# Optimization experiments

Measured on AMD Instinct MI355X. Metric: run time of the kernel, lower is better.

## Reference

```python
import jax, jax.numpy as jnp
import numpy as np

N_NODES = 10000
N_EDGES = 320000
NFEAT, NHID, NCLASS = 512, 256, 40


def setup_inputs() -> dict:
    key = jax.random.key(0)
    ks = jax.random.split(key, 8)
    x = jax.random.normal(ks[0], (N_NODES, NFEAT), dtype=jnp.float32)
    edge_src = jax.random.randint(ks[1], (N_EDGES,), 0, N_NODES, dtype=jnp.int32)
    edge_dst = jax.random.randint(ks[2], (N_EDGES,), 0, N_NODES, dtype=jnp.int32)
    edge_w = jax.random.uniform(ks[3], (N_EDGES,), dtype=jnp.float32)
    W1 = jax.random.normal(ks[4], (NFEAT, NHID), dtype=jnp.float32) * (1.0 / np.sqrt(NFEAT))
    b1 = jax.random.normal(ks[5], (NHID,), dtype=jnp.float32) * 0.01
    W2 = jax.random.normal(ks[6], (NHID, NCLASS), dtype=jnp.float32) * (1.0 / np.sqrt(NHID))
    b2 = jax.random.normal(ks[7], (NCLASS,), dtype=jnp.float32) * 0.01
    return {"x": x, "edge_src": edge_src, "edge_dst": edge_dst, "edge_w": edge_w,
            "W1": W1, "b1": b1, "W2": W2, "b2": b2}


def _spmm(edge_src, edge_dst, edge_w, h):
    # out[i] = sum_{e: dst_e == i} w_e * h[src_e]   (sparse adj @ h)
    msgs = h[edge_src] * edge_w[:, None]            # [E, d]
    return jax.ops.segment_sum(msgs, edge_dst, num_segments=h.shape[0])


def reference(x, edge_src, edge_dst, edge_w, W1, b1, W2, b2):
    # Layer 1: GraphConvolution(nfeat->nhid) with ReLU (dropout = identity in eval)
    h = jax.nn.relu(_spmm(edge_src, edge_dst, edge_w, x @ W1) + b1)
    # Layer 2: GraphConvolution(nhid->nclass), identity activation
    out = _spmm(edge_src, edge_dst, edge_w, h @ W2) + b2
    return jax.nn.log_softmax(out, axis=1)
```

## Files before the change

### kernel.cpp

```cpp
#include <hip/hip_runtime.h>
#include <hip/hip_bf16.h>
#include <math.h>

#define N_NODES 10000
#define MPAD    10112
#define N_EDGES 320000
#define NFEAT   512
#define NHID    256
#define NCLASS  40
#define SLOT    96
#define EB      ((N_EDGES + 255) / 256)
#define G1X     (MPAD / 128)
#define NG1     (G1X * (NHID / 128))

typedef short  short8  __attribute__((ext_vector_type(8)));
typedef float  floatx4 __attribute__((ext_vector_type(4)));

__device__ __forceinline__ unsigned short f2b(float f) {
  __hip_bfloat16 h = __float2bfloat16(f);
  unsigned short u; __builtin_memcpy(&u, &h, 2); return u;
}
__device__ __forceinline__ float b2f(unsigned short u) {
  return __uint_as_float(((unsigned)u) << 16);
}
__device__ __forceinline__ short8 pack8(float4 a, float4 b) {
  short8 r;
  r[0] = (short)f2b(a.x); r[1] = (short)f2b(a.y); r[2] = (short)f2b(a.z); r[3] = (short)f2b(a.w);
  r[4] = (short)f2b(b.x); r[5] = (short)f2b(b.y); r[6] = (short)f2b(b.z); r[7] = (short)f2b(b.w);
  return r;
}


__global__ __launch_bounds__(256) void prep_k(const float* __restrict__ W1,
                                              const float* __restrict__ W2,
                                              unsigned short* __restrict__ w1t,
                                              unsigned short* __restrict__ w2t,
                                              int* __restrict__ cnt) {
  int tid = blockIdx.x * 256 + threadIdx.x;
  if (tid < N_NODES) cnt[tid] = 0;
  const int nw1 = NFEAT * NHID;
  if (tid < nw1) {
    int k = tid / NHID, n = tid % NHID;
    w1t[n * NFEAT + k] = f2b(W1[tid]);
  } else {
    int j = tid - nw1;
    if (j < 64 * NHID) {
      int n = j >> 8;
      int k = j & 255;
      w2t[j] = (n < NCLASS) ? f2b(W2[k * NCLASS + n]) : (unsigned short)0;
    }
  }
}


__global__ __launch_bounds__(256) void gemm1_scatter_k(
    const float* __restrict__ x, const unsigned short* __restrict__ w1t,
    unsigned short* __restrict__ xw1b,
    const int* __restrict__ src, const int* __restrict__ dst,
    const float* __restrict__ w, int* __restrict__ cnt, int2* __restrict__ epk) {
  if (blockIdx.x >= NG1) {
    int e = (blockIdx.x - NG1) * 256 + threadIdx.x;
    if (e < N_EDGES) {
      int d = dst[e];
      int p = atomicAdd(&cnt[d], 1);
      int2 pk; pk.x = src[e]; pk.y = __float_as_int(w[e]);
      epk[d * SLOT + p] = pk;
    }
    return;
  }
  __shared__ short8 As[128 * 4];
  __shared__ short8 Bs[128 * 4];

  const int b  = blockIdx.x;
  const int bx = b % G1X;
  const int by = b / G1X;
  const int bm = bx * 128;
  const int bn = by * 128;
  const int t  = threadIdx.x;
  const int l  = t & 63;
  const int wv = t >> 6;
  const int wr = wv >> 1, wc = wv & 1;

  const int rowX = t >> 1;
  const int sX   = (t & 1) * 2;

  const floatx4 zero = {0.f, 0.f, 0.f, 0.f};
  floatx4 acc[4][4];
#pragma unroll
  for (int mi = 0; mi < 4; mi++)
#pragma unroll
    for (int ni = 0; ni < 4; ni++) acc[mi][ni] = zero;

  const int q = l >> 4;

  for (int k0 = 0; k0 < NFEAT; k0 += 32) {
    int arow = bm + rowX;
    float4 xa0 = make_float4(0.f, 0.f, 0.f, 0.f), xa1 = xa0, xa2 = xa0, xa3 = xa0;
    if (arow < N_NODES) {
      const float* xp = &x[(size_t)arow * NFEAT + k0 + sX * 8];
      xa0 = *(const float4*)(xp);
      xa1 = *(const float4*)(xp + 4);
      xa2 = *(const float4*)(xp + 8);
      xa3 = *(const float4*)(xp + 12);
    }
    short8 a0 = pack8(xa0, xa1), a1 = pack8(xa2, xa3);
    short8 b0 = *(const short8*)&w1t[(size_t)(bn + rowX) * NFEAT + k0 + sX * 8];
    short8 b1v = *(const short8*)&w1t[(size_t)(bn + rowX) * NFEAT + k0 + sX * 8 + 8];
    __syncthreads();
    As[rowX * 4 + ((sX    ) ^ (rowX & 3))] = a0;
    As[rowX * 4 + ((sX + 1) ^ (rowX & 3))] = a1;
    Bs[rowX * 4 + ((sX    ) ^ (rowX & 3))] = b0;
    Bs[rowX * 4 + ((sX + 1) ^ (rowX & 3))] = b1v;
    __syncthreads();

    short8 af[4], bf[4];
#pragma unroll
    for (int mi = 0; mi < 4; mi++) {
      int ar = wr * 64 + mi * 16 + (l & 15);
      af[mi] = As[ar * 4 + (q ^ (ar & 3))];
    }
#pragma unroll
    for (int ni = 0; ni < 4; ni++) {
      int bc = wc * 64 + ni * 16 + (l & 15);
      bf[ni] = Bs[bc * 4 + (q ^ (bc & 3))];
    }
#pragma unroll
    for (int mi = 0; mi < 4; mi++)
#pragma unroll
      for (int ni = 0; ni < 4; ni++)
        acc[mi][ni] = __builtin_amdgcn_mfma_f32_16x16x32_bf16(af[mi], bf[ni], acc[mi][ni], 0, 0, 0);
  }

#pragma unroll
  for (int mi = 0; mi < 4; mi++)
#pragma unroll
    for (int ni = 0; ni < 4; ni++) {
      int row = bm + wr * 64 + mi * 16 + (l >> 4) * 4;
      int col = bn + wc * 64 + ni * 16 + (l & 15);
#pragma unroll
      for (int r = 0; r < 4; r++)
        xw1b[(size_t)(row + r) * NHID + col] = f2b(acc[mi][ni][r]);
    }
}


__global__ __launch_bounds__(256) void spmm1_k(const int* __restrict__ cnt,
                                               const int2* __restrict__ epk,
                                               const unsigned short* __restrict__ xw1b,
                                               const float* __restrict__ b1,
                                               unsigned short* __restrict__ h) {
  int bid     = blockIdx.x;
  int xcd     = bid & 7;
  int slice   = xcd >> 2;
  int quarter = xcd & 3;
  int wave    = threadIdx.x >> 6;
  int lane    = threadIdx.x & 63;
  int node    = (bid >> 3) * 4 + wave + quarter * 2500;
  int hh      = lane >> 5;
  int f       = lane & 31;
  int fbase   = slice * 128 + f * 4;

  int e0 = node * SLOT;
  int n  = cnt[node];
  float a0 = 0.f, a1 = 0.f, a2 = 0.f, a3 = 0.f;
  for (int base = 0; base < n; base += 64) {
    int c2 = n - base; if (c2 > 64) c2 = 64;
    int2 my = make_int2(0, 0);
    if (lane < c2) my = epk[e0 + base + lane];
    int j = 0;
    for (; j + 8 <= c2; j += 8) {
#pragma unroll
      for (int p = 0; p < 4; p++) {
        int   idx = j + 2 * p + hh;
        int   s   = __shfl(my.x, idx);
        float wj  = __int_as_float(__shfl(my.y, idx));
        uint2 v = *(const uint2*)&xw1b[(size_t)s * NHID + fbase];
        a0 = fmaf(wj, b2f((unsigned short)(v.x & 0xffff)), a0);
        a1 = fmaf(wj, b2f((unsigned short)(v.x >> 16)),    a1);
        a2 = fmaf(wj, b2f((unsigned short)(v.y & 0xffff)), a2);
        a3 = fmaf(wj, b2f((unsigned short)(v.y >> 16)),    a3);
      }
    }
    for (; j < c2; j++) {
      int   s  = __shfl(my.x, j);
      float wj = __int_as_float(__shfl(my.y, j));
      if (hh == 0) {
        uint2 v = *(const uint2*)&xw1b[(size_t)s * NHID + fbase];
        a0 = fmaf(wj, b2f((unsigned short)(v.x & 0xffff)), a0);
        a1 = fmaf(wj, b2f((unsigned short)(v.x >> 16)),    a1);
        a2 = fmaf(wj, b2f((unsigned short)(v.y & 0xffff)), a2);
        a3 = fmaf(wj, b2f((unsigned short)(v.y >> 16)),    a3);
      }
    }
  }
  a0 += __shfl_xor(a0, 32);
  a1 += __shfl_xor(a1, 32);
  a2 += __shfl_xor(a2, 32);
  a3 += __shfl_xor(a3, 32);
  if (hh == 0) {
    a0 = fmaxf(a0 + b1[fbase + 0], 0.f);
    a1 = fmaxf(a1 + b1[fbase + 1], 0.f);
    a2 = fmaxf(a2 + b1[fbase + 2], 0.f);
    a3 = fmaxf(a3 + b1[fbase + 3], 0.f);
    uint2 po;
    po.x = ((unsigned)f2b(a1) << 16) | f2b(a0);
    po.y = ((unsigned)f2b(a3) << 16) | f2b(a2);
    *(uint2*)&h[(size_t)node * NHID + fbase] = po;
  }
}


__global__ __launch_bounds__(256) void gemm2_k(const unsigned short* __restrict__ h,
                                               const unsigned short* __restrict__ w2t,
                                               float* __restrict__ hw2) {
  __shared__ short8 As[64 * 4];
  __shared__ short8 Bs[64 * 4];

  const int t  = threadIdx.x;
  const int bm = blockIdx.x * 64;
  const int l  = t & 63;
  const int wv = t >> 6;
  const int wr = wv >> 1, wc = wv & 1;
  const int srow = t >> 2, sslot = t & 3;

  const floatx4 zero = {0.f, 0.f, 0.f, 0.f};
  floatx4 acc[2][2];
  acc[0][0] = zero; acc[0][1] = zero; acc[1][0] = zero; acc[1][1] = zero;

  const int q = l >> 4;

  for (int k0 = 0; k0 < NHID; k0 += 32) {
    short8 av = *(const short8*)&h  [(size_t)(bm + srow) * NHID + k0 + sslot * 8];
    short8 bv = *(const short8*)&w2t[(size_t)srow * NHID + k0 + sslot * 8];
    __syncthreads();
    As[srow * 4 + (sslot ^ (srow & 3))] = av;
    Bs[srow * 4 + (sslot ^ (srow & 3))] = bv;
    __syncthreads();

    short8 af[2], bf2[2];
#pragma unroll
    for (int mi = 0; mi < 2; mi++) {
      int ar = wr * 32 + mi * 16 + (l & 15);
      af[mi] = As[ar * 4 + (q ^ (ar & 3))];
    }
#pragma unroll
    for (int ni = 0; ni < 2; ni++) {
      int bc = wc * 32 + ni * 16 + (l & 15);
      bf2[ni] = Bs[bc * 4 + (q ^ (bc & 3))];
    }
#pragma unroll
    for (int mi = 0; mi < 2; mi++)
#pragma unroll
      for (int ni = 0; ni < 2; ni++)
        acc[mi][ni] = __builtin_amdgcn_mfma_f32_16x16x32_bf16(af[mi], bf2[ni], acc[mi][ni], 0, 0, 0);
  }

#pragma unroll
  for (int mi = 0; mi < 2; mi++)
#pragma unroll
    for (int ni = 0; ni < 2; ni++) {
      int row = bm + wr * 32 + mi * 16 + (l >> 4) * 4;
      int col = wc * 32 + ni * 16 + (l & 15);
#pragma unroll
      for (int r = 0; r < 4; r++)
        hw2[(size_t)(row + r) * 64 + col] = acc[mi][ni][r];
    }
}


__global__ __launch_bounds__(256) void spmm2_k(const int* __restrict__ cnt,
                                               const int2* __restrict__ epk,
                                               const float* __restrict__ hw2,
                                               const float* __restrict__ b2,
                                               float* __restrict__ out) {
  int wave = threadIdx.x >> 6;
  int lane = threadIdx.x & 63;
  int i    = blockIdx.x * 4 + wave;
  int hh   = lane >> 5;
  int c    = lane & 31;
  bool act = (c * 2 < NCLASS);
  int e0 = i * SLOT;
  int n  = cnt[i];
  float a0 = 0.f, a1 = 0.f;
  for (int base = 0; base < n; base += 64) {
    int c2 = n - base; if (c2 > 64) c2 = 64;
    int2 my = make_int2(0, 0);
    if (lane < c2) my = epk[e0 + base + lane];
    int j = 0;
    for (; j + 8 <= c2; j += 8) {
#pragma unroll
      for (int p = 0; p < 4; p++) {
        int   idx = j + 2 * p + hh;
        int   s   = __shfl(my.x, idx);
        float wj  = __int_as_float(__shfl(my.y, idx));
        float2 v = *(const float2*)&hw2[(size_t)s * 64 + c * 2];
        a0 = fmaf(wj, v.x, a0);
        a1 = fmaf(wj, v.y, a1);
      }
    }
    for (; j < c2; j++) {
      int   s  = __shfl(my.x, j);
      float wj = __int_as_float(__shfl(my.y, j));
      if (hh == 0) {
        float2 v = *(const float2*)&hw2[(size_t)s * 64 + c * 2];
        a0 = fmaf(wj, v.x, a0);
        a1 = fmaf(wj, v.y, a1);
      }
    }
  }
  a0 += __shfl_xor(a0, 32);
  a1 += __shfl_xor(a1, 32);
  if (act) { a0 += b2[c * 2]; a1 += b2[c * 2 + 1]; }
  float mv = act ? fmaxf(a0, a1) : -INFINITY;
#pragma unroll
  for (int o = 16; o > 0; o >>= 1) mv = fmaxf(mv, __shfl_xor(mv, o));
  float ex = act ? (expf(a0 - mv) + expf(a1 - mv)) : 0.f;
#pragma unroll
  for (int o = 16; o > 0; o >>= 1) ex += __shfl_xor(ex, o);
  float ls = logf(ex);
  if (act && hh == 0) {
    float2 o2; o2.x = a0 - mv - ls; o2.y = a1 - mv - ls;
    *(float2*)&out[(size_t)i * NCLASS + c * 2] = o2;
  }
}


static inline size_t align256(size_t v) { return (v + 255) & ~(size_t)255; }

extern "C" void kernel_launch(void* const* d_in, const int* in_sizes, int n_in,
                              void* d_out, int out_size, void* d_ws, size_t ws_size,
                              hipStream_t stream) {
  const float* x        = (const float*)d_in[0];
  const int*   edge_src = (const int*)  d_in[1];
  const int*   edge_dst = (const int*)  d_in[2];
  const float* edge_w   = (const float*)d_in[3];
  const float* W1       = (const float*)d_in[4];
  const float* b1       = (const float*)d_in[5];
  const float* W2       = (const float*)d_in[6];
  const float* b2       = (const float*)d_in[7];
  float* out = (float*)d_out;

  char* ws = (char*)d_ws;
  size_t off = 0;
  unsigned short* w1t  = (unsigned short*)(ws + off); off = align256(off + (size_t)NFEAT * NHID * 2);
  unsigned short* w2t  = (unsigned short*)(ws + off); off = align256(off + (size_t)64 * NHID * 2);
  unsigned short* xw1b = (unsigned short*)(ws + off); off = align256(off + (size_t)MPAD * NHID * 2);
  unsigned short* h    = (unsigned short*)(ws + off); off = align256(off + (size_t)MPAD * NHID * 2);
  float* hw2 = (float*)(ws + off); off = align256(off + (size_t)MPAD * 64 * 4);
  int*   cnt = (int*)  (ws + off); off = align256(off + (size_t)N_NODES * 4);
  int2*  epk = (int2*) (ws + off); off = align256(off + (size_t)N_NODES * SLOT * 8);

  const int PREP_ITEMS = NFEAT * NHID + 64 * NHID;
  prep_k<<<(PREP_ITEMS + 255) / 256, 256, 0, stream>>>(W1, W2, w1t, w2t, cnt);

  gemm1_scatter_k<<<NG1 + EB, 256, 0, stream>>>(x, w1t, xw1b,
                                                edge_src, edge_dst, edge_w, cnt, epk);

  spmm1_k<<<5000, 256, 0, stream>>>(cnt, epk, xw1b, b1, h);

  gemm2_k<<<157, 256, 0, stream>>>(h, w2t, hw2);

  spmm2_k<<<2500, 256, 0, stream>>>(cnt, epk, hw2, b2, out);
}
```

Baseline: 78.55 us.

## Split edge scatter from GEMM1, pad atomic counters, double-buffer smaller GEMM tiles

Moves the edge scatter out of the fused GEMM1 launch into its own 1024-thread kernel. Per-node counters are padded to a 64-byte stride to reduce atomic contention and false sharing. GEMM1 now uses 64x128 tiles with double-buffered shared memory and register prefetch of the next K-slice, so one barrier per iteration replaces two and more blocks are launched. In exchange there is an extra kernel launch, the scatter no longer overlaps with GEMM work, and prep_k now launches over the larger padded counter range.

```diff
diff --git a/kernel.cpp b/kernel.cpp
--- a/kernel.cpp
+++ b/kernel.cpp
@@ -9,9 +9,8 @@
 #define NHID    256
 #define NCLASS  40
 #define SLOT    96
-#define EB      ((N_EDGES + 255) / 256)
-#define G1X     (MPAD / 128)
-#define NG1     (G1X * (NHID / 128))
+#define CSTRIDE 16
+#define NBM1    158
 
 typedef short  short8  __attribute__((ext_vector_type(8)));
 typedef float  floatx4 __attribute__((ext_vector_type(4)));
@@ -37,106 +36,115 @@
                                               unsigned short* __restrict__ w2t,
                                               int* __restrict__ cnt) {
   int tid = blockIdx.x * 256 + threadIdx.x;
-  if (tid < N_NODES) cnt[tid] = 0;
+  if (tid < N_NODES * CSTRIDE) cnt[tid] = 0;
   const int nw1 = NFEAT * NHID;
   if (tid < nw1) {
     int k = tid / NHID, n = tid % NHID;
     w1t[n * NFEAT + k] = f2b(W1[tid]);
-  } else {
+  } else if (tid < nw1 + 64 * NHID) {
     int j = tid - nw1;
-    if (j < 64 * NHID) {
-      int n = j >> 8;
-      int k = j & 255;
-      w2t[j] = (n < NCLASS) ? f2b(W2[k * NCLASS + n]) : (unsigned short)0;
-    }
-  }
-}
-
-
-__global__ __launch_bounds__(256) void gemm1_scatter_k(
-    const float* __restrict__ x, const unsigned short* __restrict__ w1t,
-    unsigned short* __restrict__ xw1b,
-    const int* __restrict__ src, const int* __restrict__ dst,
-    const float* __restrict__ w, int* __restrict__ cnt, int2* __restrict__ epk) {
-  if (blockIdx.x >= NG1) {
-    int e = (blockIdx.x - NG1) * 256 + threadIdx.x;
-    if (e < N_EDGES) {
-      int d = dst[e];
-      int p = atomicAdd(&cnt[d], 1);
-      int2 pk; pk.x = src[e]; pk.y = __float_as_int(w[e]);
-      epk[d * SLOT + p] = pk;
-    }
-    return;
-  }
-  __shared__ short8 As[128 * 4];
-  __shared__ short8 Bs[128 * 4];
-
-  const int b  = blockIdx.x;
-  const int bx = b % G1X;
-  const int by = b / G1X;
-  const int bm = bx * 128;
-  const int bn = by * 128;
+    int n = j >> 8;
+    int k = j & 255;
+    w2t[j] = (n < NCLASS) ? f2b(W2[k * NCLASS + n]) : (unsigned short)0;
+  }
+}
+
+
+__global__ __launch_bounds__(1024) void scatter_k(const int* __restrict__ src,
+                                                  const int* __restrict__ dst,
+                                                  const float* __restrict__ w,
+                                                  int* __restrict__ cnt,
+                                                  int2* __restrict__ epk) {
+  int e = blockIdx.x * 1024 + threadIdx.x;
+  if (e < N_EDGES) {
+    int d = dst[e];
+    int p = atomicAdd(&cnt[d << 4], 1);
+    int2 pk; pk.x = src[e]; pk.y = __float_as_int(w[e]);
+    epk[d * SLOT + p] = pk;
+  }
+}
+
+
+__global__ __launch_bounds__(256) void gemm1_k(const float* __restrict__ x,
+                                               const unsigned short* __restrict__ w1t,
+                                               unsigned short* __restrict__ xw1b) {
+  __shared__ short8 As[2][64 * 4];
+  __shared__ short8 Bs[2][128 * 4];
+
   const int t  = threadIdx.x;
   const int l  = t & 63;
-  const int wv = t >> 6;
-  const int wr = wv >> 1, wc = wv & 1;
-
-  const int rowX = t >> 1;
-  const int sX   = (t & 1) * 2;
-
+  const int wc = t >> 6;
+  const int bm = (blockIdx.x % NBM1) * 64;
+  const int bn = (blockIdx.x / NBM1) * 128;
+
+  const int rowA = t >> 2, sA = t & 3;
+  const int rowB = t >> 1, sB = (t & 1) * 2;
+
+  const float4 z4 = make_float4(0.f, 0.f, 0.f, 0.f);
   const floatx4 zero = {0.f, 0.f, 0.f, 0.f};
-  floatx4 acc[4][4];
+  floatx4 acc[4][2];
+#pragma unroll
+  for (int mi = 0; mi < 4; mi++) { acc[mi][0] = zero; acc[mi][1] = zero; }
+
+  const int q = l >> 4;
+  const bool arok = (bm + rowA) < N_NODES;
+  const float* xrow = &x[(size_t)(bm + rowA) * NFEAT + sA * 8];
+  const unsigned short* brow = &w1t[(size_t)(bn + rowB) * NFEAT + sB * 8];
+
+  {
+    float4 a0 = z4, a1 = z4;
+    if (arok) { a0 = *(const float4*)(xrow); a1 = *(const float4*)(xrow + 4); }
+    short8 b0 = *(const short8*)(brow);
+    short8 b1 = *(const short8*)(brow + 8);
+    As[0][rowA * 4 + (sA ^ (rowA & 3))] = pack8(a0, a1);
+    Bs[0][rowB * 4 + ((sB    ) ^ (rowB & 3))] = b0;
+    Bs[0][rowB * 4 + ((sB + 1) ^ (rowB & 3))] = b1;
+  }
+
+  for (int s = 0; s < 16; s++) {
+    __syncthreads();
+    const int cur = s & 1;
+    float4 na0 = z4, na1 = z4;
+    short8 nb0, nb1;
+    const bool more = (s < 15);
+    if (more) {
+      const int k1 = (s + 1) * 32;
+      if (arok) { na0 = *(const float4*)(xrow + k1); na1 = *(const float4*)(xrow + k1 + 4); }
+      nb0 = *(const short8*)(brow + k1);
+      nb1 = *(const short8*)(brow + k1 + 8);
+    }
+
+    short8 af[4], bf[2];
+#pragma unroll
+    for (int mi = 0; mi < 4; mi++) {
+      int ar = mi * 16 + (l & 15);
+      af[mi] = As[cur][ar * 4 + (q ^ (ar & 3))];
+    }
+#pragma unroll
+    for (int ni = 0; ni < 2; ni++) {
+      int bc = wc * 32 + ni * 16 + (l & 15);
+      bf[ni] = Bs[cur][bc * 4 + (q ^ (bc & 3))];
+    }
+#pragma unroll
+    for (int mi = 0; mi < 4; mi++)
+#pragma unroll
+      for (int ni = 0; ni < 2; ni++)
+        acc[mi][ni] = __builtin_amdgcn_mfma_f32_16x16x32_bf16(af[mi], bf[ni], acc[mi][ni], 0, 0, 0);
+
+    if (more) {
+      const int nxt = cur ^ 1;
+      As[nxt][rowA * 4 + (sA ^ (rowA & 3))] = pack8(na0, na1);
+      Bs[nxt][rowB * 4 + ((sB    ) ^ (rowB & 3))] = nb0;
+      Bs[nxt][rowB * 4 + ((sB + 1) ^ (rowB & 3))] = nb1;
+    }
+  }
+
 #pragma unroll
   for (int mi = 0; mi < 4; mi++)
 #pragma unroll
-    for (int ni = 0; ni < 4; ni++) acc[mi][ni] = zero;
-
-  const int q = l >> 4;
-
-  for (int k0 = 0; k0 < NFEAT; k0 += 32) {
-    int arow = bm + rowX;
-    float4 xa0 = make_float4(0.f, 0.f, 0.f, 0.f), xa1 = xa0, xa2 = xa0, xa3 = xa0;
-    if (arow < N_NODES) {
-      const float* xp = &x[(size_t)arow * NFEAT + k0 + sX * 8];
-      xa0 = *(const float4*)(xp);
-      xa1 = *(const float4*)(xp + 4);
-      xa2 = *(const float4*)(xp + 8);
-      xa3 = *(const float4*)(xp + 12);
-    }
-    short8 a0 = pack8(xa0, xa1), a1 = pack8(xa2, xa3);
-    short8 b0 = *(const short8*)&w1t[(size_t)(bn + rowX) * NFEAT + k0 + sX * 8];
-    short8 b1v = *(const short8*)&w1t[(size_t)(bn + rowX) * NFEAT + k0 + sX * 8 + 8];
-    __syncthreads();
-    As[rowX * 4 + ((sX    ) ^ (rowX & 3))] = a0;
-    As[rowX * 4 + ((sX + 1) ^ (rowX & 3))] = a1;
-    Bs[rowX * 4 + ((sX    ) ^ (rowX & 3))] = b0;
-    Bs[rowX * 4 + ((sX + 1) ^ (rowX & 3))] = b1v;
-    __syncthreads();
-
-    short8 af[4], bf[4];
-#pragma unroll
-    for (int mi = 0; mi < 4; mi++) {
-      int ar = wr * 64 + mi * 16 + (l & 15);
-      af[mi] = As[ar * 4 + (q ^ (ar & 3))];
-    }
-#pragma unroll
-    for (int ni = 0; ni < 4; ni++) {
-      int bc = wc * 64 + ni * 16 + (l & 15);
-      bf[ni] = Bs[bc * 4 + (q ^ (bc & 3))];
-    }
-#pragma unroll
-    for (int mi = 0; mi < 4; mi++)
-#pragma unroll
-      for (int ni = 0; ni < 4; ni++)
-        acc[mi][ni] = __builtin_amdgcn_mfma_f32_16x16x32_bf16(af[mi], bf[ni], acc[mi][ni], 0, 0, 0);
-  }
-
-#pragma unroll
-  for (int mi = 0; mi < 4; mi++)
-#pragma unroll
-    for (int ni = 0; ni < 4; ni++) {
-      int row = bm + wr * 64 + mi * 16 + (l >> 4) * 4;
-      int col = bn + wc * 64 + ni * 16 + (l & 15);
+    for (int ni = 0; ni < 2; ni++) {
+      int row = bm + mi * 16 + (l >> 4) * 4;
+      int col = bn + wc * 32 + ni * 16 + (l & 15);
 #pragma unroll
       for (int r = 0; r < 4; r++)
         xw1b[(size_t)(row + r) * NHID + col] = f2b(acc[mi][ni][r]);
@@ -161,7 +169,7 @@
   int fbase   = slice * 128 + f * 4;
 
   int e0 = node * SLOT;
-  int n  = cnt[node];
+  int n  = cnt[node << 4];
   float a0 = 0.f, a1 = 0.f, a2 = 0.f, a3 = 0.f;
   for (int base = 0; base < n; base += 64) {
     int c2 = n - base; if (c2 > 64) c2 = 64;
@@ -280,7 +288,7 @@
   int c    = lane & 31;
   bool act = (c * 2 < NCLASS);
   int e0 = i * SLOT;
-  int n  = cnt[i];
+  int n  = cnt[i << 4];
   float a0 = 0.f, a1 = 0.f;
   for (int base = 0; base < n; base += 64) {
     int c2 = n - base; if (c2 > 64) c2 = 64;
@@ -347,14 +355,15 @@
   unsigned short* xw1b = (unsigned short*)(ws + off); off = align256(off + (size_t)MPAD * NHID * 2);
   unsigned short* h    = (unsigned short*)(ws + off); off = align256(off + (size_t)MPAD * NHID * 2);
   float* hw2 = (float*)(ws + off); off = align256(off + (size_t)MPAD * 64 * 4);
-  int*   cnt = (int*)  (ws + off); off = align256(off + (size_t)N_NODES * 4);
+  int*   cnt = (int*)  (ws + off); off = align256(off + (size_t)N_NODES * CSTRIDE * 4);
   int2*  epk = (int2*) (ws + off); off = align256(off + (size_t)N_NODES * SLOT * 8);
 
-  const int PREP_ITEMS = NFEAT * NHID + 64 * NHID;
+  const int PREP_ITEMS = N_NODES * CSTRIDE;
   prep_k<<<(PREP_ITEMS + 255) / 256, 256, 0, stream>>>(W1, W2, w1t, w2t, cnt);
 
-  gemm1_scatter_k<<<NG1 + EB, 256, 0, stream>>>(x, w1t, xw1b,
-                                                edge_src, edge_dst, edge_w, cnt, epk);
+  scatter_k<<<(N_EDGES + 1023) / 1024, 1024, 0, stream>>>(edge_src, edge_dst, edge_w, cnt, epk);
+
+  gemm1_k<<<NBM1 * 2, 256, 0, stream>>>(x, w1t, xw1b);
 
   spmm1_k<<<5000, 256, 0, stream>>>(cnt, epk, xw1b, b1, h);
 
```

Result: faster. 76.46 us (-2.7%).
